# Performance work log

Measured on AMD Instinct MI355X. Metric: run time of the kernel, lower is better.

The kernel has to match this reference:

```python
import jax, jax.numpy as jnp
import numpy as np

# Hard-coded electrode groupings from the torch module
REGIONS = [[0, 1, 16, 17], [2, 18, 19], [3, 4], [20], [7, 8], [21, 25, 26], [5, 22],
           [6, 23, 24], [9, 27], [11], [29], [10, 15, 28], [12, 30], [13, 14, 31]]
R = 14          # number of regions
T = 4           # max region length (ragged lens 1..4, padded)
LENS = np.array([len(r) for r in REGIONS])
REG_IDX = np.array([r + [r[-1]] * (T - len(r)) for r in REGIONS])   # [R,T] padded gather indices
LAST_IDX = np.array([r[-1] for r in REGIONS])                        # last electrode per region
MASKS = (np.arange(T)[:, None] < LENS[None, :])                      # [T,R] valid-step mask

B, E, H = 8192, 128, 128   # batch, eeg_size, hidden per direction (output_size=2H=256)
G = 4 * H                  # gate width (i,f,g,o)


def setup_inputs() -> dict:
    key = jax.random.key(0)
    ks = jax.random.split(key, 5)
    s = 1.0 / np.sqrt(H)   # matches torch LSTM uniform(-1/sqrt(H),1/sqrt(H)) scale
    return {
        "x": jax.random.normal(ks[0], (B, 32, E), jnp.float32),
        "w_ih": jax.random.normal(ks[1], (R, 2, G, E), jnp.float32) * s,
        "w_hh": jax.random.normal(ks[2], (R, 2, G, H), jnp.float32) * s,
        "b_ih": jax.random.normal(ks[3], (R, 2, G), jnp.float32) * s,
        "b_hh": jax.random.normal(ks[4], (R, 2, G), jnp.float32) * s,
        "gamma": jnp.ones((R,), jnp.float32),
        "beta": jnp.zeros((R,), jnp.float32),
    }


def _cell(x_t, h, c, W_ih, W_hh, b):
    # x_t:[B,R,E] h,c:[B,R,H] W_ih:[R,G,E] W_hh:[R,G,H] b:[R,G]; torch gate order i,f,g,o
    gates = jnp.einsum('bre,rge->brg', x_t, W_ih) + jnp.einsum('brh,rgh->brg', h, W_hh) + b
    i, f, g, o = jnp.split(gates, 4, axis=-1)
    c_new = jax.nn.sigmoid(f) * c + jax.nn.sigmoid(i) * jnp.tanh(g)
    h_new = jax.nn.sigmoid(o) * jnp.tanh(c_new)
    return h_new, c_new


def reference(x, w_ih, w_hh, b_ih, b_hh, gamma, beta):
    xs = x[:, jnp.asarray(REG_IDX), :]              # [B,R,T,E] per-region gather (padded)
    xs_t = jnp.transpose(xs, (2, 0, 1, 3))          # [T,B,R,E]
    masks = jnp.asarray(MASKS)                      # [T,R]
    bf = b_ih[:, 0] + b_hh[:, 0]
    bb = b_ih[:, 1] + b_hh[:, 1]
    h0 = jnp.zeros((x.shape[0], R, H), x.dtype)
    c0 = h0

    # Forward direction: scan over padded time, freeze state past each region's length
    def step(carry, inp):
        h, c = carry
        x_t, m = inp
        h_n, c_n = _cell(x_t, h, c, w_ih[:, 0], w_hh[:, 0], bf)
        m_ = m[None, :, None]
        return (jnp.where(m_, h_n, h), jnp.where(m_, c_n, c)), None

    (h_fwd, _), _ = jax.lax.scan(step, (h0, c0), (xs_t, masks))

    # Backward direction output at last timestep == exactly one backward step on the last element
    x_last = x[:, jnp.asarray(LAST_IDX), :]         # [B,R,E]
    h_bwd, _ = _cell(x_last, h0, c0, w_ih[:, 1], w_hh[:, 1], bb)

    out = jnp.concatenate([h_fwd, h_bwd], axis=-1)  # [B,R,2H] == [batch, regions, output_size]

    # BatchNorm1d(num_features=R), training mode: biased var over (batch, feature)
    mean = out.mean(axis=(0, 2), keepdims=True)
    var = out.var(axis=(0, 2), keepdims=True)
    xhat = (out - mean) * jax.lax.rsqrt(var + 1e-5)
    return gamma[None, :, None] * xhat + beta[None, :, None]
```

## Files before the change

### kernel.cpp

```cpp
#include <hip/hip_runtime.h>

typedef __attribute__((ext_vector_type(8))) _Float16 half8;
typedef __attribute__((ext_vector_type(16))) float f32x16;

static __device__ const int d_LENS[14] = {4,3,2,1,2,3,2,3,2,1,1,3,2,3};
static __device__ const int d_RIDX[14][4] = {
  {0,1,16,17},{2,18,19,19},{3,4,4,4},{20,20,20,20},{7,8,8,8},{21,25,26,26},
  {5,22,22,22},{6,23,24,24},{9,27,27,27},{11,11,11,11},{29,29,29,29},
  {10,15,28,28},{12,30,30,30},{13,14,31,31}};

static __device__ const int d_nTot[8] = {64,96,96,128,128,128,128,128};
static __device__ const int d_regA[8] = {0,1,5,7,11,13,2,6};
static __device__ const int d_regB[8] = {0,12,12,3,9,10,4,8};
static __device__ const int d_boff[8] = {0,0,32,0,0,0,0,0};

__device__ __forceinline__ float sigf(float v){
  return __builtin_amdgcn_rcpf(1.0f + __expf(-v));
}
__device__ __forceinline__ float tanhf2(float v){
  return 1.0f - 2.0f*__builtin_amdgcn_rcpf(1.0f + __expf(2.0f*v));
}

__device__ __forceinline__ void gload16(const void* g, void* l){
  __builtin_amdgcn_global_load_lds((const __attribute__((address_space(1))) void*)g,
                                   (__attribute__((address_space(3))) void*)l, 16, 0, 0);
}

__device__ __forceinline__ void stage_chunk(const _Float16* __restrict__ base, int ci,
                                            char* wb, int tid){
  const char* src = (const char*)base + (size_t)ci*65536;
  #pragma unroll
  for (int i=0;i<8;i++){
    int L = i*8192 + tid*16;
    gload16(src + L, wb + L);
  }
}

__global__ void prep_w(const float* __restrict__ w_ih, const float* __restrict__ w_hh,
                       const float* __restrict__ b_ih, const float* __restrict__ b_hh,
                       _Float16* __restrict__ wih, _Float16* __restrict__ whh,
                       float* __restrict__ bias)
{
  int tid = blockIdx.x*256 + threadIdx.x;
  if (tid < 458752){
    int a = (tid >= 229376);
    const float* src = a ? w_hh : w_ih;
    _Float16* dst    = a ? whh  : wih;
    int t = (a ? (tid - 229376) : tid) * 8;
    int l  = (t>>3)&63, ks=(t>>9)&7, g=(t>>12)&3, uu=(t>>14)&1, c=(t>>15)&1, rd=t>>16;
    int v = l&31, q = l>>5;
    int n  = g*128 + c*64 + uu*32 + v;
    int k0 = q*8 + ks*16;
    const float* s = src + (size_t)rd*65536 + n*128 + k0;
    float4 a0 = *(const float4*)s;
    float4 a1 = *(const float4*)(s+4);
    half8 h;
    h[0]=(_Float16)a0.x; h[1]=(_Float16)a0.y; h[2]=(_Float16)a0.z; h[3]=(_Float16)a0.w;
    h[4]=(_Float16)a1.x; h[5]=(_Float16)a1.y; h[6]=(_Float16)a1.z; h[7]=(_Float16)a1.w;
    *(half8*)(dst + t) = h;
  } else {
    int t = tid - 458752;
    if (t < 14336){
      int rd = t >> 9, np = t & 511;
      int c = (np >> 8) & 1, uu = (np >> 7) & 1, g = (np >> 5) & 3, vv = np & 31;
      int n = g*128 + c*64 + uu*32 + vv;
      bias[t] = b_ih[rd*512 + n] + b_hh[rd*512 + n];
    }
  }
}

__global__ void prep_x(const float* __restrict__ x, _Float16* __restrict__ x16)
{
  size_t i8 = (size_t)blockIdx.x*256 + threadIdx.x;
  int l    = (int)(i8 & 63);
  int ks   = (int)((i8 >> 6) & 7);
  int wr   = (int)((i8 >> 9) & 3);
  int chan = (int)((i8 >> 11) & 31);
  size_t bt = i8 >> 16;
  int row = (int)(bt*128) + wr*32 + (l & 31);
  int k0  = (l >> 5)*8 + ks*16;
  const float* s = x + ((size_t)row*32 + chan)*128 + k0;
  float4 a0 = *(const float4*)s;
  float4 a1 = *(const float4*)(s+4);
  half8 h;
  h[0]=(_Float16)a0.x; h[1]=(_Float16)a0.y; h[2]=(_Float16)a0.z; h[3]=(_Float16)a0.w;
  h[4]=(_Float16)a1.x; h[5]=(_Float16)a1.y; h[6]=(_Float16)a1.z; h[7]=(_Float16)a1.w;
  *(half8*)(x16 + i8*8) = h;
}

template<int XMODE, int F16OUT>
__global__ __launch_bounds__(512, 1) void lstm_k(
    const float* __restrict__ xf32, const _Float16* __restrict__ x16,
    const _Float16* __restrict__ wih, const _Float16* __restrict__ whh,
    const float* __restrict__ bias,
    _Float16* __restrict__ hout, float* __restrict__ fout,
    float* __restrict__ part)
{
  __shared__ char wb[65536];
  __shared__ char hb0[65536];
  __shared__ float red[16];

  const int tid  = threadIdx.x;
  const int lane = tid & 63;
  const int wv = tid >> 6;
  const int wr = wv >> 1;
  const int u  = wv & 1;
  const int v  = lane & 31;
  const int q  = lane >> 5;

  const int xcd = blockIdx.x & 7;
  const int kk  = blockIdx.x >> 3;
  if (kk >= d_nTot[xcd]) return;
  int r, bt;
  if (kk < 64){ r = d_regA[xcd]; bt = kk; }
  else        { r = d_regB[xcd]; bt = d_boff[xcd] + (kk - 64); }
  const int b0 = bt << 7;
  const int len = d_LENS[r];

  float bf[2][4];
  #pragma unroll
  for (int c=0;c<2;c++)
    #pragma unroll
    for (int g=0;g<4;g++)
      bf[c][g] = bias[(size_t)r*1024 + c*256 + u*128 + g*32 + v];

  float cst[2][16];
  #pragma unroll
  for (int c=0;c<2;c++)
    #pragma unroll
    for (int e=0;e<16;e++) cst[c][e] = 0.0f;

  half8 xa0,xa1,xa2,xa3,xa4,xa5,xa6,xa7;
  float lsum = 0.0f, lsq = 0.0f;
  const int hrow = wr*32 + v;
  char* const wp = wb + ((u*32)<<10) + (lane<<4);

#define SB() __builtin_amdgcn_sched_barrier(0)
#define GXS(KS, AR) { \
    half8 b0 = *(const half8*)(wp + ((0*8+KS)<<10)); \
    half8 b1 = *(const half8*)(wp + ((1*8+KS)<<10)); \
    half8 b2 = *(const half8*)(wp + ((2*8+KS)<<10)); \
    half8 b3 = *(const half8*)(wp + ((3*8+KS)<<10)); \
    acc0 = __builtin_amdgcn_mfma_f32_32x32x16_f16(AR, b0, acc0, 0,0,0); \
    acc1 = __builtin_amdgcn_mfma_f32_32x32x16_f16(AR, b1, acc1, 0,0,0); \
    acc2 = __builtin_amdgcn_mfma_f32_32x32x16_f16(AR, b2, acc2, 0,0,0); \
    acc3 = __builtin_amdgcn_mfma_f32_32x32x16_f16(AR, b3, acc3, 0,0,0); }
#define HXS(KS) { \
    half8 ah = *(const half8*)(hbr + ((hrow*256 + KS*32 + q*16) ^ ((hrow&15)<<4))); \
    half8 b0 = *(const half8*)(wp + ((0*8+KS)<<10)); \
    half8 b1 = *(const half8*)(wp + ((1*8+KS)<<10)); \
    half8 b2 = *(const half8*)(wp + ((2*8+KS)<<10)); \
    half8 b3 = *(const half8*)(wp + ((3*8+KS)<<10)); \
    acc0 = __builtin_amdgcn_mfma_f32_32x32x16_f16(ah, b0, acc0, 0,0,0); \
    acc1 = __builtin_amdgcn_mfma_f32_32x32x16_f16(ah, b1, acc1, 0,0,0); \
    acc2 = __builtin_amdgcn_mfma_f32_32x32x16_f16(ah, b2, acc2, 0,0,0); \
    acc3 = __builtin_amdgcn_mfma_f32_32x32x16_f16(ah, b3, acc3, 0,0,0); }

  for (int t=0; t<len; ++t){
    const int chan = d_RIDX[r][t];
    if (XMODE){
      const _Float16* xp = x16 + (((size_t)bt*32 + chan)*4 + wr)*4096 + lane*8;
      xa0 = *(const half8*)(xp);          xa1 = *(const half8*)(xp + 512);
      xa2 = *(const half8*)(xp + 1024);   xa3 = *(const half8*)(xp + 1536);
      xa4 = *(const half8*)(xp + 2048);   xa5 = *(const half8*)(xp + 2560);
      xa6 = *(const half8*)(xp + 3072);   xa7 = *(const half8*)(xp + 3584);
    } else {
      const float* xb = xf32 + (((size_t)(b0 + wr*32 + v))*32 + chan)*128 + q*8;
      #define LXF(DST, OFF) { \
        float4 a0 = *(const float4*)(xb + OFF); \
        float4 a1 = *(const float4*)(xb + OFF + 4); \
        half8 a; \
        a[0]=(_Float16)a0.x; a[1]=(_Float16)a0.y; a[2]=(_Float16)a0.z; a[3]=(_Float16)a0.w; \
        a[4]=(_Float16)a1.x; a[5]=(_Float16)a1.y; a[6]=(_Float16)a1.z; a[7]=(_Float16)a1.w; \
        DST = a; }
      LXF(xa0,0) LXF(xa1,16) LXF(xa2,32) LXF(xa3,48)
      LXF(xa4,64) LXF(xa5,80) LXF(xa6,96) LXF(xa7,112)
      #undef LXF
    }
    const bool last = (t == len-1);
    char* hbr = hb0 + (((t+1)&1) << 15);
    char* hbw = hb0 + ((t&1) << 15);

    #pragma unroll
    for (int c=0;c<2;c++){
      f32x16 acc0, acc1, acc2, acc3;
      #pragma unroll
      for (int e=0;e<16;e++){
        acc0[e] = bf[c][0]; acc1[e] = bf[c][1];
        acc2[e] = bf[c][2]; acc3[e] = bf[c][3];
      }

      __syncthreads();
      stage_chunk(wih, r*4 + c, wb, tid);
      __syncthreads();
      GXS(0,xa0) GXS(1,xa1) SB();
      GXS(2,xa2) GXS(3,xa3) SB();
      GXS(4,xa4) GXS(5,xa5) SB();
      GXS(6,xa6) GXS(7,xa7) SB();
      if (t > 0){
        __syncthreads();
        stage_chunk(whh, r*4 + c, wb, tid);
        __syncthreads();
        HXS(0) HXS(1) SB();
        HXS(2) HXS(3) SB();
        HXS(4) HXS(5) SB();
        HXS(6) HXS(7) SB();
      }
      const int ccol = c*64 + u*32 + v;
      #pragma unroll
      for (int e=0;e<16;e++){
        float iv = acc0[e], fv = acc1[e];
        float gv = acc2[e], ov = acc3[e];
        float cn = sigf(iv)*tanhf2(gv) + sigf(fv)*cst[c][e];
        cst[c][e] = cn;
        float hv = sigf(ov)*tanhf2(cn);
        _Float16 hh = (_Float16)hv;
        int rl = wr*32 + (e&3) + ((e>>2)<<3) + (q<<2);
        *(_Float16*)(hbw + ((rl*256 + ccol*2) ^ ((rl&15)<<4))) = hh;
        if (last){
          float hr = (float)hh;
          lsum += hr; lsq += hr*hr;
        }
      }
    }
  }

  {
    char* hbk = hb0 + ((len&1) << 15);
    #pragma unroll
    for (int c=0;c<2;c++){
      f32x16 acc0, acc1, acc2, acc3;
      {
        float g0 = bias[(size_t)r*1024 + 512 + c*256 + u*128 + 0*32 + v];
        float g1 = bias[(size_t)r*1024 + 512 + c*256 + u*128 + 1*32 + v];
        float g2 = bias[(size_t)r*1024 + 512 + c*256 + u*128 + 2*32 + v];
        float g3 = bias[(size_t)r*1024 + 512 + c*256 + u*128 + 3*32 + v];
        #pragma unroll
        for (int e=0;e<16;e++){
          acc0[e] = g0; acc1[e] = g1; acc2[e] = g2; acc3[e] = g3;
        }
      }
      __syncthreads();
      stage_chunk(wih, r*4 + 2 + c, wb, tid);
      __syncthreads();
      GXS(0,xa0) GXS(1,xa1) SB();
      GXS(2,xa2) GXS(3,xa3) SB();
      GXS(4,xa4) GXS(5,xa5) SB();
      GXS(6,xa6) GXS(7,xa7) SB();
      const int ccol = c*64 + u*32 + v;
      #pragma unroll
      for (int e=0;e<16;e++){
        float iv = acc0[e];
        float gv = acc2[e], ov = acc3[e];
        float cn = sigf(iv)*tanhf2(gv);
        float hv = sigf(ov)*tanhf2(cn);
        _Float16 hh = (_Float16)hv;
        int rl = wr*32 + (e&3) + ((e>>2)<<3) + (q<<2);
        *(_Float16*)(hbk + ((rl*256 + ccol*2) ^ ((rl&15)<<4))) = hh;
        float hr = (float)hh;
        lsum += hr; lsq += hr*hr;
      }
    }
  }
#undef GXS
#undef HXS
#undef SB

  __syncthreads();
  {
    const char* hf  = hb0 + (((len-1)&1) << 15);
    const char* hbk = hb0 + ((len&1) << 15);
    #pragma unroll
    for (int i=0;i<4;i++){
      int row = (tid>>4) + i*32;
      int bo  = (tid&15)*16;
      int lp  = row*256 + (bo ^ ((row&15)<<4));
      uint4 df = *(const uint4*)(hf + lp);
      uint4 db = *(const uint4*)(hbk + lp);
      size_t ob = ((size_t)(b0+row)*14 + r)*256;
      if (F16OUT){
        *(uint4*)((char*)hout + ob*2 + bo)       = df;
        *(uint4*)((char*)hout + ob*2 + 256 + bo) = db;
      } else {
        const _Float16* pf = (const _Float16*)&df;
        const _Float16* pb = (const _Float16*)&db;
        float* of  = fout + ob + (bo>>1);
        float* obw = fout + ob + 128 + (bo>>1);
        float4 o0, o1;
        o0.x=(float)pf[0]; o0.y=(float)pf[1]; o0.z=(float)pf[2]; o0.w=(float)pf[3];
        o1.x=(float)pf[4]; o1.y=(float)pf[5]; o1.z=(float)pf[6]; o1.w=(float)pf[7];
        *(float4*)of = o0; *(float4*)(of+4) = o1;
        o0.x=(float)pb[0]; o0.y=(float)pb[1]; o0.z=(float)pb[2]; o0.w=(float)pb[3];
        o1.x=(float)pb[4]; o1.y=(float)pb[5]; o1.z=(float)pb[6]; o1.w=(float)pb[7];
        *(float4*)obw = o0; *(float4*)(obw+4) = o1;
      }
    }
  }

  #pragma unroll
  for (int off=32; off>0; off>>=1){
    lsum += __shfl_down(lsum, off);
    lsq  += __shfl_down(lsq, off);
  }
  __syncthreads();
  if (lane == 0){ red[wv] = lsum; red[8+wv] = lsq; }
  __syncthreads();
  if (tid == 0){
    float s = 0.0f, s2 = 0.0f;
    #pragma unroll
    for (int ww=0;ww<8;ww++){ s += red[ww]; s2 += red[8+ww]; }
    part[((size_t)r*64 + bt)*2]     = s;
    part[((size_t)r*64 + bt)*2 + 1] = s2;
  }
}

__global__ void stats_k(const float* __restrict__ part, const float* __restrict__ gamma,
                        const float* __restrict__ beta, float* __restrict__ stat)
{
  int r = blockIdx.x, l = threadIdx.x;
  float s  = part[((size_t)r*64 + l)*2];
  float s2 = part[((size_t)r*64 + l)*2 + 1];
  #pragma unroll
  for (int off=32; off>0; off>>=1){ s += __shfl_down(s, off); s2 += __shfl_down(s2, off); }
  if (l == 0){
    const float cnt = 2097152.0f;
    float m = s / cnt;
    float var = s2 / cnt - m*m;
    float rstd = rsqrtf(var + 1e-5f);
    float sc = gamma[r]*rstd;
    stat[r*2]   = sc;
    stat[r*2+1] = beta[r] - m*sc;
  }
}

__global__ void apply_f16(const _Float16* __restrict__ hst, const float* __restrict__ stat,
                          float* __restrict__ out)
{
  size_t i8 = (size_t)blockIdx.x*256 + threadIdx.x;
  uint4 vv = *(const uint4*)(hst + i8*8);
  int r = (int)((i8 >> 5) % 14);
  float sc = stat[r*2], sh = stat[r*2+1];
  const _Float16* hp = (const _Float16*)&vv;
  float4 o0, o1;
  o0.x = (float)hp[0]*sc + sh; o0.y = (float)hp[1]*sc + sh;
  o0.z = (float)hp[2]*sc + sh; o0.w = (float)hp[3]*sc + sh;
  o1.x = (float)hp[4]*sc + sh; o1.y = (float)hp[5]*sc + sh;
  o1.z = (float)hp[6]*sc + sh; o1.w = (float)hp[7]*sc + sh;
  ((float4*)out)[i8*2]     = o0;
  ((float4*)out)[i8*2 + 1] = o1;
}

__global__ void apply_f32(float* __restrict__ out, const float* __restrict__ stat)
{
  size_t idx = (size_t)blockIdx.x*256 + threadIdx.x;
  float4* p = (float4*)out + idx;
  float4 vv = *p;
  int r = (int)((idx >> 6) % 14);
  float sc = stat[r*2], sh = stat[r*2+1];
  vv.x = vv.x*sc + sh; vv.y = vv.y*sc + sh; vv.z = vv.z*sc + sh; vv.w = vv.w*sc + sh;
  *p = vv;
}

extern "C" void kernel_launch(void* const* d_in, const int* in_sizes, int n_in,
                              void* d_out, int out_size, void* d_ws, size_t ws_size,
                              hipStream_t stream)
{
  const float* x     = (const float*)d_in[0];
  const float* w_ih  = (const float*)d_in[1];
  const float* w_hh  = (const float*)d_in[2];
  const float* b_ih  = (const float*)d_in[3];
  const float* b_hh  = (const float*)d_in[4];
  const float* gamma = (const float*)d_in[5];
  const float* beta  = (const float*)d_in[6];
  float* out = (float*)d_out;

  const size_t HS = 29360128;
  const size_t XS = 33554432;
  const size_t wbytes = (size_t)1835008*2;
  const size_t tail = (14336 + 1792 + 28)*4;
  const size_t need_full = XS*2 + HS*2 + 2*wbytes + tail;

  char* wsp = (char*)d_ws;
  int full = (ws_size >= need_full) ? 1 : 0;

  _Float16* x16p; _Float16* hstore; _Float16* wihp;
  if (full){
    x16p   = (_Float16*)wsp;
    hstore = (_Float16*)(wsp + XS*2);
    wihp   = (_Float16*)(wsp + XS*2 + HS*2);
  } else {
    x16p   = (_Float16*)wsp;
    hstore = (_Float16*)wsp;
    wihp   = (_Float16*)wsp;
  }
  _Float16* whhp = wihp + 1835008;
  float* biasp = (float*)(whhp + 1835008);
  float* partp = biasp + 14336;
  float* statp = partp + 1792;

  prep_w<<<1848, 256, 0, stream>>>(w_ih, w_hh, b_ih, b_hh, wihp, whhp, biasp);
  if (full){
    prep_x<<<16384, 256, 0, stream>>>(x, x16p);
    lstm_k<1,1><<<1024, 512, 0, stream>>>(x, x16p, wihp, whhp, biasp,
                                          hstore, out, partp);
  } else {
    lstm_k<0,0><<<1024, 512, 0, stream>>>(x, x16p, wihp, whhp, biasp,
                                          hstore, out, partp);
  }
  stats_k<<<14, 64, 0, stream>>>(partp, gamma, beta, statp);
  if (full)
    apply_f16<<<14336, 256, 0, stream>>>(hstore, statp, out);
  else
    apply_f32<<<28672, 256, 0, stream>>>(out, statp);
}
```

Before: 402.9 us.

## Overlap LSTM gate epilogue with staging of the next weight chunk

Restructures the per-step loop into a software pipeline. The pointwise gate math and h writes for one column chunk now run while the next weight chunk is being staged into shared memory, in the window between the two barriers, instead of after the last MFMA. This hides the global-to-LDS load latency behind the sigmoid/tanh work. The cost is that the chunk-1 accumulators must stay live across loop iterations, which raises register pressure, and the control flow and state handoff become harder to follow.

```diff
diff --git a/kernel.cpp b/kernel.cpp
--- a/kernel.cpp
+++ b/kernel.cpp
@@ -131,6 +131,7 @@
     for (int e=0;e<16;e++) cst[c][e] = 0.0f;
 
   half8 xa0,xa1,xa2,xa3,xa4,xa5,xa6,xa7;
+  f32x16 acc0, acc1, acc2, acc3;
   float lsum = 0.0f, lsq = 0.0f;
   const int hrow = wr*32 + v;
   char* const wp = wb + ((u*32)<<10) + (lane<<4);
@@ -155,6 +156,33 @@
     acc1 = __builtin_amdgcn_mfma_f32_32x32x16_f16(ah, b1, acc1, 0,0,0); \
     acc2 = __builtin_amdgcn_mfma_f32_32x32x16_f16(ah, b2, acc2, 0,0,0); \
     acc3 = __builtin_amdgcn_mfma_f32_32x32x16_f16(ah, b3, acc3, 0,0,0); }
+#define ACCI(CC) { \
+    float g0 = bf[CC][0], g1 = bf[CC][1], g2 = bf[CC][2], g3 = bf[CC][3]; \
+    _Pragma("unroll") for (int e=0;e<16;e++){ \
+      acc0[e]=g0; acc1[e]=g1; acc2[e]=g2; acc3[e]=g3; } }
+#define PWF(C, HB, LAST) { \
+    const int ccol = C*64 + u*32 + v; \
+    _Pragma("unroll") for (int e=0;e<16;e++){ \
+      float iv = acc0[e], fv = acc1[e]; \
+      float gv = acc2[e], ov = acc3[e]; \
+      float cn = sigf(iv)*tanhf2(gv) + sigf(fv)*cst[C][e]; \
+      cst[C][e] = cn; \
+      float hv = sigf(ov)*tanhf2(cn); \
+      _Float16 hh = (_Float16)hv; \
+      int rl = wr*32 + (e&3) + ((e>>2)<<3) + (q<<2); \
+      *(_Float16*)((HB) + ((rl*256 + ccol*2) ^ ((rl&15)<<4))) = hh; \
+      if (LAST){ float hr = (float)hh; lsum += hr; lsq += hr*hr; } } }
+#define PWB(C, HB) { \
+    const int ccol = C*64 + u*32 + v; \
+    _Pragma("unroll") for (int e=0;e<16;e++){ \
+      float iv = acc0[e]; \
+      float gv = acc2[e], ov = acc3[e]; \
+      float cn = sigf(iv)*tanhf2(gv); \
+      float hv = sigf(ov)*tanhf2(cn); \
+      _Float16 hh = (_Float16)hv; \
+      int rl = wr*32 + (e&3) + ((e>>2)<<3) + (q<<2); \
+      *(_Float16*)((HB) + ((rl*256 + ccol*2) ^ ((rl&15)<<4))) = hh; \
+      float hr = (float)hh; lsum += hr; lsq += hr*hr; } }
 
   for (int t=0; t<len; ++t){
     const int chan = d_RIDX[r][t];
@@ -181,89 +209,86 @@
     char* hbr = hb0 + (((t+1)&1) << 15);
     char* hbw = hb0 + ((t&1) << 15);
 
-    #pragma unroll
-    for (int c=0;c<2;c++){
-      f32x16 acc0, acc1, acc2, acc3;
+    __syncthreads();
+    stage_chunk(wih, r*4 + 0, wb, tid);
+    if (t > 0) PWF(1, hbr, false)
+    __syncthreads();
+    ACCI(0)
+    GXS(0,xa0) GXS(1,xa1) SB();
+    GXS(2,xa2) GXS(3,xa3) SB();
+    GXS(4,xa4) GXS(5,xa5) SB();
+    GXS(6,xa6) GXS(7,xa7) SB();
+    if (t > 0){
+      __syncthreads();
+      stage_chunk(whh, r*4 + 0, wb, tid);
+      __syncthreads();
+      HXS(0) HXS(1) SB();
+      HXS(2) HXS(3) SB();
+      HXS(4) HXS(5) SB();
+      HXS(6) HXS(7) SB();
+    }
+    __syncthreads();
+    stage_chunk(wih, r*4 + 1, wb, tid);
+    PWF(0, hbw, last)
+    __syncthreads();
+    ACCI(1)
+    GXS(0,xa0) GXS(1,xa1) SB();
+    GXS(2,xa2) GXS(3,xa3) SB();
+    GXS(4,xa4) GXS(5,xa5) SB();
+    GXS(6,xa6) GXS(7,xa7) SB();
+    if (t > 0){
+      __syncthreads();
+      stage_chunk(whh, r*4 + 1, wb, tid);
+      __syncthreads();
+      HXS(0) HXS(1) SB();
+      HXS(2) HXS(3) SB();
+      HXS(4) HXS(5) SB();
+      HXS(6) HXS(7) SB();
+    }
+  }
+
+  {
+    char* hfin = hb0 + (((len-1)&1) << 15);
+    char* hbk  = hb0 + ((len&1) << 15);
+    __syncthreads();
+    stage_chunk(wih, r*4 + 2, wb, tid);
+    PWF(1, hfin, true)
+    __syncthreads();
+    {
+      float g0 = bias[(size_t)r*1024 + 512 + 0*256 + u*128 + 0*32 + v];
+      float g1 = bias[(size_t)r*1024 + 512 + 0*256 + u*128 + 1*32 + v];
+      float g2 = bias[(size_t)r*1024 + 512 + 0*256 + u*128 + 2*32 + v];
+      float g3 = bias[(size_t)r*1024 + 512 + 0*256 + u*128 + 3*32 + v];
       #pragma unroll
-      for (int e=0;e<16;e++){
-        acc0[e] = bf[c][0]; acc1[e] = bf[c][1];
-        acc2[e] = bf[c][2]; acc3[e] = bf[c][3];
-      }
-
-      __syncthreads();
-      stage_chunk(wih, r*4 + c, wb, tid);
-      __syncthreads();
-      GXS(0,xa0) GXS(1,xa1) SB();
-      GXS(2,xa2) GXS(3,xa3) SB();
-      GXS(4,xa4) GXS(5,xa5) SB();
-      GXS(6,xa6) GXS(7,xa7) SB();
-      if (t > 0){
-        __syncthreads();
-        stage_chunk(whh, r*4 + c, wb, tid);
-        __syncthreads();
-        HXS(0) HXS(1) SB();
-        HXS(2) HXS(3) SB();
-        HXS(4) HXS(5) SB();
-        HXS(6) HXS(7) SB();
-      }
-      const int ccol = c*64 + u*32 + v;
+      for (int e=0;e<16;e++){ acc0[e]=g0; acc1[e]=g1; acc2[e]=g2; acc3[e]=g3; }
+    }
+    GXS(0,xa0) GXS(1,xa1) SB();
+    GXS(2,xa2) GXS(3,xa3) SB();
+    GXS(4,xa4) GXS(5,xa5) SB();
+    GXS(6,xa6) GXS(7,xa7) SB();
+    __syncthreads();
+    stage_chunk(wih, r*4 + 3, wb, tid);
+    PWB(0, hbk)
+    __syncthreads();
+    {
+      float g0 = bias[(size_t)r*1024 + 512 + 1*256 + u*128 + 0*32 + v];
+      float g1 = bias[(size_t)r*1024 + 512 + 1*256 + u*128 + 1*32 + v];
+      float g2 = bias[(size_t)r*1024 + 512 + 1*256 + u*128 + 2*32 + v];
+      float g3 = bias[(size_t)r*1024 + 512 + 1*256 + u*128 + 3*32 + v];
       #pragma unroll
-      for (int e=0;e<16;e++){
-        float iv = acc0[e], fv = acc1[e];
-        float gv = acc2[e], ov = acc3[e];
-        float cn = sigf(iv)*tanhf2(gv) + sigf(fv)*cst[c][e];
-        cst[c][e] = cn;
-        float hv = sigf(ov)*tanhf2(cn);
-        _Float16 hh = (_Float16)hv;
-        int rl = wr*32 + (e&3) + ((e>>2)<<3) + (q<<2);
-        *(_Float16*)(hbw + ((rl*256 + ccol*2) ^ ((rl&15)<<4))) = hh;
-        if (last){
-          float hr = (float)hh;
-          lsum += hr; lsq += hr*hr;
-        }
-      }
-    }
-  }
-
-  {
-    char* hbk = hb0 + ((len&1) << 15);
-    #pragma unroll
-    for (int c=0;c<2;c++){
-      f32x16 acc0, acc1, acc2, acc3;
-      {
-        float g0 = bias[(size_t)r*1024 + 512 + c*256 + u*128 + 0*32 + v];
-        float g1 = bias[(size_t)r*1024 + 512 + c*256 + u*128 + 1*32 + v];
-        float g2 = bias[(size_t)r*1024 + 512 + c*256 + u*128 + 2*32 + v];
-        float g3 = bias[(size_t)r*1024 + 512 + c*256 + u*128 + 3*32 + v];
-        #pragma unroll
-        for (int e=0;e<16;e++){
-          acc0[e] = g0; acc1[e] = g1; acc2[e] = g2; acc3[e] = g3;
-        }
-      }
-      __syncthreads();
-      stage_chunk(wih, r*4 + 2 + c, wb, tid);
-      __syncthreads();
-      GXS(0,xa0) GXS(1,xa1) SB();
-      GXS(2,xa2) GXS(3,xa3) SB();
-      GXS(4,xa4) GXS(5,xa5) SB();
-      GXS(6,xa6) GXS(7,xa7) SB();
-      const int ccol = c*64 + u*32 + v;
-      #pragma unroll
-      for (int e=0;e<16;e++){
-        float iv = acc0[e];
-        float gv = acc2[e], ov = acc3[e];
-        float cn = sigf(iv)*tanhf2(gv);
-        float hv = sigf(ov)*tanhf2(cn);
-        _Float16 hh = (_Float16)hv;
-        int rl = wr*32 + (e&3) + ((e>>2)<<3) + (q<<2);
-        *(_Float16*)(hbk + ((rl*256 + ccol*2) ^ ((rl&15)<<4))) = hh;
-        float hr = (float)hh;
-        lsum += hr; lsq += hr*hr;
-      }
-    }
+      for (int e=0;e<16;e++){ acc0[e]=g0; acc1[e]=g1; acc2[e]=g2; acc3[e]=g3; }
+    }
+    GXS(0,xa0) GXS(1,xa1) SB();
+    GXS(2,xa2) GXS(3,xa3) SB();
+    GXS(4,xa4) GXS(5,xa5) SB();
+    GXS(6,xa6) GXS(7,xa7) SB();
+    PWB(1, hbk)
   }
 #undef GXS
 #undef HXS
+#undef ACCI
+#undef PWF
+#undef PWB
 #undef SB
 
   __syncthreads();
```

Measured after the change: 391.6 us. 1.03x faster.
